# Performance work log

Measured on AMD Instinct MI355X. Metric: run time of the kernel, lower is better.

Reference implementation:

```python
import jax, jax.numpy as jnp
import numpy as np

NEG = -9e15  # kept for fidelity though mask is unused in original forward

def setup_inputs() -> dict:
    key = jax.random.key(0)
    k1, k2, k3 = jax.random.split(key, 3)
    N, Fin, Fout = 8192, 512, 256
    x = jax.random.normal(k1, (N, Fin), dtype=jnp.float32)
    # xavier_uniform with gain=1.414 ~ U(-b, b), b = gain*sqrt(6/(fan_in+fan_out))
    bW = 1.414 * np.sqrt(6.0 / (Fin + Fout))
    W = jax.random.uniform(k2, (Fin, Fout), minval=-bW, maxval=bW, dtype=jnp.float32)
    ba = 1.414 * np.sqrt(6.0 / (2 * Fout + 1))
    a = jax.random.uniform(k3, (2 * Fout, 1), minval=-ba, maxval=ba, dtype=jnp.float32)
    return {"x": x, "W": W, "a": a}

def reference(x, W, a):
    # h: [N, Fout]
    h = x @ W
    Fout = h.shape[1]
    # Algebraic decomposition of additive score: e_ij = relu(a1.h_i + a2.h_j)
    a1, a2 = a[:Fout, 0], a[Fout:, 0]  # [Fout], [Fout]
    f = h @ a1  # [N] contribution of row node i
    g = h @ a2  # [N] contribution of col node j
    e = jax.nn.relu(f[:, None] + g[None, :])  # [N, N]
    attention = jax.nn.softmax(e, axis=1)
    h_prime = attention @ h  # [N, Fout]
    return jax.nn.elu(h_prime)
```

## Files before the change

### kernel.cpp

```cpp
#include <hip/hip_runtime.h>
#include <math.h>

#define NROWS 8192
#define FIN   512
#define FOUT  256
#define NCHUNK 512
#define CHROWS 16

typedef _Float16 f16;
typedef _Float16 f16x8 __attribute__((ext_vector_type(8)));
typedef float    f32x4 __attribute__((ext_vector_type(4)));

__global__ __launch_bounds__(256) void prep(const float* __restrict__ x,
                                            const float* __restrict__ W,
                                            f16* __restrict__ xh,
                                            f16* __restrict__ Wt,
                                            float* __restrict__ fg) {
    const int b = blockIdx.x, t = threadIdx.x;
    if (b < 256) {
        const size_t base = (size_t)b * 16384;
#pragma unroll 4
        for (int i = 0; i < 16; ++i) {
            const size_t idx = base + (size_t)i * 1024 + t * 4;
            float4 v = *(const float4*)&x[idx];
            union { f16 h[4]; ushort4 u; } cv;
            cv.h[0] = (f16)v.x; cv.h[1] = (f16)v.y;
            cv.h[2] = (f16)v.z; cv.h[3] = (f16)v.w;
            *(ushort4*)&xh[idx] = cv.u;
        }
    } else {
        const int n = b - 256;
        Wt[(size_t)n * FIN + t]       = (f16)W[(size_t)t * FOUT + n];
        Wt[(size_t)n * FIN + t + 256] = (f16)W[(size_t)(t + 256) * FOUT + n];
        if (n < 64) fg[n * 256 + t] = 0.f;
    }
}

__global__ __launch_bounds__(256) void gemm_fg(const f16* __restrict__ xh,
                                               const f16* __restrict__ Wt,
                                               const float* __restrict__ a,
                                               f16* __restrict__ h,
                                               float* __restrict__ f,
                                               float* __restrict__ g) {
    __shared__ __align__(16) f16 As[64][136];
    __shared__ __align__(16) f16 Bs[64][136];
    __shared__ float sf[2][64], sg[2][64];
    const int tid = threadIdx.x;
    const int n0 = blockIdx.x * 64;
    const int m0 = blockIdx.y * 64;
    const int srow = tid >> 2, sseg = (tid & 3) * 8;
    const int w = tid >> 6, lane = tid & 63;
    const int wm = (w & 1) * 32, wn = (w >> 1) * 32;
    const int l15 = lane & 15, quad = lane >> 4;

    f16x8 pa[4], pb[4];
#pragma unroll
    for (int j = 0; j < 4; ++j) {
        pa[j] = *(const f16x8*)&xh[(size_t)(m0 + srow) * FIN + j * 32 + sseg];
        pb[j] = *(const f16x8*)&Wt[(size_t)(n0 + srow) * FIN + j * 32 + sseg];
    }

    f32x4 acc[2][2] = {};
    for (int k0 = 0; k0 < FIN; k0 += 128) {
        __syncthreads();
#pragma unroll
        for (int j = 0; j < 4; ++j) {
            *(f16x8*)&As[srow][j * 32 + sseg] = pa[j];
            *(f16x8*)&Bs[srow][j * 32 + sseg] = pb[j];
        }
        __syncthreads();
        if (k0 + 128 < FIN) {
#pragma unroll
            for (int j = 0; j < 4; ++j) {
                pa[j] = *(const f16x8*)&xh[(size_t)(m0 + srow) * FIN + k0 + 128 + j * 32 + sseg];
                pb[j] = *(const f16x8*)&Wt[(size_t)(n0 + srow) * FIN + k0 + 128 + j * 32 + sseg];
            }
        }
#pragma unroll
        for (int kk = 0; kk < 4; ++kk) {
            f16x8 af[2], bf[2];
#pragma unroll
            for (int ti = 0; ti < 2; ++ti)
                af[ti] = *(const f16x8*)&As[wm + ti * 16 + l15][kk * 32 + quad * 8];
#pragma unroll
            for (int tj = 0; tj < 2; ++tj)
                bf[tj] = *(const f16x8*)&Bs[wn + tj * 16 + l15][kk * 32 + quad * 8];
#pragma unroll
            for (int ti = 0; ti < 2; ++ti)
#pragma unroll
                for (int tj = 0; tj < 2; ++tj)
                    acc[ti][tj] = __builtin_amdgcn_mfma_f32_16x16x32_f16(af[ti], bf[tj], acc[ti][tj], 0, 0, 0);
        }
    }
#pragma unroll
    for (int ti = 0; ti < 2; ++ti)
#pragma unroll
        for (int tj = 0; tj < 2; ++tj) {
            const int col = n0 + wn + tj * 16 + l15;
#pragma unroll
            for (int r = 0; r < 4; ++r) {
                const int row = m0 + wm + ti * 16 + quad * 4 + r;
                h[(size_t)row * FOUT + col] = (f16)acc[ti][tj][r];
            }
        }
    const float a1c0 = a[n0 + wn + l15];
    const float a1c1 = a[n0 + wn + 16 + l15];
    const float a2c0 = a[FOUT + n0 + wn + l15];
    const float a2c1 = a[FOUT + n0 + wn + 16 + l15];
    const int wnIdx = w >> 1;
#pragma unroll
    for (int ti = 0; ti < 2; ++ti) {
        float pf[4], pg[4];
#pragma unroll
        for (int r = 0; r < 4; ++r) {
            pf[r] = acc[ti][0][r] * a1c0 + acc[ti][1][r] * a1c1;
            pg[r] = acc[ti][0][r] * a2c0 + acc[ti][1][r] * a2c1;
        }
#pragma unroll
        for (int off = 8; off >= 1; off >>= 1)
#pragma unroll
            for (int r = 0; r < 4; ++r) {
                pf[r] += __shfl_xor(pf[r], off, 16);
                pg[r] += __shfl_xor(pg[r], off, 16);
            }
        if (l15 == 0)
#pragma unroll
            for (int r = 0; r < 4; ++r) {
                sf[wnIdx][wm + ti * 16 + quad * 4 + r] = pf[r];
                sg[wnIdx][wm + ti * 16 + quad * 4 + r] = pg[r];
            }
    }
    __syncthreads();
    if (tid < 64) {
        atomicAdd(&f[m0 + tid], sf[0][tid] + sf[1][tid]);
        atomicAdd(&g[m0 + tid], sg[0][tid] + sg[1][tid]);
    }
}

__global__ __launch_bounds__(256) void rank_scatter(const float* __restrict__ g,
                                                    float* __restrict__ gs,
                                                    int* __restrict__ perm) {
    const int t = threadIdx.x;
    const int jl = t & 31;
    const int seg = t >> 5;
    const int j = blockIdx.x * 32 + jl;
    const float gj = g[j];
    const int base = seg * (NROWS / 8);
    int cnt = 0;
    for (int r = 0; r < NROWS / 8; r += 4) {
        const float4 v = *(const float4*)&g[base + r];
        const int i0 = base + r;
        cnt += (v.x < gj) || (v.x == gj && (i0 + 0) < j);
        cnt += (v.y < gj) || (v.y == gj && (i0 + 1) < j);
        cnt += (v.z < gj) || (v.z == gj && (i0 + 2) < j);
        cnt += (v.w < gj) || (v.w == gj && (i0 + 3) < j);
    }
    __shared__ int part[8][32];
    part[seg][jl] = cnt;
    __syncthreads();
    if (seg == 0) {
        int rank = 0;
#pragma unroll
        for (int s = 0; s < 8; ++s) rank += part[s][jl];
        gs[rank] = gj;
        perm[rank] = j;
    }
}

__global__ __launch_bounds__(256) void scan_pass1(const f16* __restrict__ h,
                                                  const int* __restrict__ perm,
                                                  const float* __restrict__ gs,
                                                  const float* __restrict__ f,
                                                  float* __restrict__ c0,
                                                  float* __restrict__ c1,
                                                  float* __restrict__ c1s,
                                                  int* __restrict__ n0arr) {
    const int b = blockIdx.x, c = threadIdx.x;
    if (b < NCHUNK) {
        const int base = b * CHROWS;
        __shared__ int p[CHROWS];
        __shared__ float wl[CHROWS];
        if (c < CHROWS) {
            p[c] = perm[base + c];
            wl[c] = expf(gs[base + c] - gs[NROWS - 1]);
        }
        __syncthreads();
        float s0 = 0.f, s1 = 0.f;
        for (int r = 0; r < CHROWS; ++r) {
            float v = (float)h[(size_t)p[r] * FOUT + c];
            s0 += v;
            s1 += wl[r] * v;
        }
        c0[b * FOUT + c] = s0;
        c1[b * FOUT + c] = s1;
        if (c == 0) {
            float t = 0.f;
            for (int r = 0; r < CHROWS; ++r) t += wl[r];
            c1s[b] = t;
        }
    } else {
        const int i = (b - NCHUNK) * 256 + c;
        const float tt = -f[i];
        int lo = 0, hi = NROWS;
        while (lo < hi) {
            int mid = (lo + hi) >> 1;
            if (gs[mid] <= tt) lo = mid + 1; else hi = mid;
        }
        n0arr[i] = lo;
    }
}

__global__ __launch_bounds__(256) void scan_pass2(const float* __restrict__ c0,
                                                  const float* __restrict__ c1,
                                                  const float* __restrict__ c1s,
                                                  float* __restrict__ o0,
                                                  float* __restrict__ o1,
                                                  float* __restrict__ o1s) {
    const int b = blockIdx.x, t = threadIdx.x;
    __shared__ float sb[256];
    if (b < 256) {
        const float e0 = c0[(2 * t) * FOUT + b];
        const float e1 = c0[(2 * t + 1) * FOUT + b];
        const float local = e0 + e1;
        sb[t] = local;
        __syncthreads();
        for (int off = 1; off < 256; off <<= 1) {
            float add = (t >= off) ? sb[t - off] : 0.f;
            __syncthreads();
            sb[t] += add;
            __syncthreads();
        }
        const float ex = sb[t] - local;
        o0[(2 * t) * FOUT + b] = ex;
        o0[(2 * t + 1) * FOUT + b] = ex + e0;
    } else if (b < 512) {
        const int col = b - 256;
        const float e0 = c1[(2 * t) * FOUT + col];
        const float e1 = c1[(2 * t + 1) * FOUT + col];
        const float local = e0 + e1;
        sb[t] = local;
        __syncthreads();
        for (int off = 1; off < 256; off <<= 1) {
            float add = (t + off < 256) ? sb[t + off] : 0.f;
            __syncthreads();
            sb[t] += add;
            __syncthreads();
        }
        const float exs = sb[t] - local;
        o1[(2 * t) * FOUT + col] = exs + e1;
        o1[(2 * t + 1) * FOUT + col] = exs;
    } else {
        const float e0 = c1s[2 * t];
        const float e1 = c1s[2 * t + 1];
        const float local = e0 + e1;
        sb[t] = local;
        __syncthreads();
        for (int off = 1; off < 256; off <<= 1) {
            float add = (t + off < 256) ? sb[t + off] : 0.f;
            __syncthreads();
            sb[t] += add;
            __syncthreads();
        }
        const float exs = sb[t] - local;
        o1s[2 * t] = exs + e1;
        o1s[2 * t + 1] = exs;
    }
}

__global__ __launch_bounds__(256) void scan_pass3(const f16* __restrict__ h,
                                                  const int* __restrict__ perm,
                                                  const float* __restrict__ gs,
                                                  const float* __restrict__ o0,
                                                  const float* __restrict__ o1,
                                                  const float* __restrict__ o1s,
                                                  f16* __restrict__ P0,
                                                  f16* __restrict__ S1,
                                                  float* __restrict__ S1s) {
    const int k = blockIdx.x, c = threadIdx.x;
    const int base = k * CHROWS;
    __shared__ int p[CHROWS];
    __shared__ float wl[CHROWS];
    if (c < CHROWS) {
        p[c] = perm[base + c];
        wl[c] = expf(gs[base + c] - gs[NROWS - 1]);
    }
    __syncthreads();
    float run0 = o0[k * FOUT + c];
    for (int r = 0; r < CHROWS; ++r) {
        P0[(size_t)(base + r) * FOUT + c] = (f16)run0;
        run0 += (float)h[(size_t)p[r] * FOUT + c];
    }
    float run1 = o1[k * FOUT + c];
    for (int r = CHROWS - 1; r >= 0; --r) {
        run1 += wl[r] * (float)h[(size_t)p[r] * FOUT + c];
        S1[(size_t)(base + r) * FOUT + c] = (f16)run1;
    }
    if (c == 0) {
        float rs = o1s[k];
        for (int r = CHROWS - 1; r >= 0; --r) { rs += wl[r]; S1s[base + r] = rs; }
    }
    if (k == NCHUNK - 1) {
        P0[(size_t)NROWS * FOUT + c] = (f16)run0;
        S1[(size_t)NROWS * FOUT + c] = (f16)0.f;
        if (c == 0) S1s[NROWS] = 0.f;
    }
}

__global__ __launch_bounds__(256) void final_kernel(const float* __restrict__ f,
                                                    const float* __restrict__ gs,
                                                    const int* __restrict__ n0arr,
                                                    const f16* __restrict__ P0,
                                                    const f16* __restrict__ S1,
                                                    const float* __restrict__ S1s,
                                                    float* __restrict__ out) {
    const int b = blockIdx.x, c = threadIdx.x;
    const float gm = gs[NROWS - 1];
#pragma unroll
    for (int rr = 0; rr < 4; ++rr) {
        const int i = b * 4 + rr;
        const float fi = f[i];
        const int n0 = n0arr[i];
        const float m = fmaxf(0.f, fi + gm);
        const float A = expf(-m);
        const float B = expf(fi + gm - m);
        const float denom = A * (float)n0 + B * S1s[n0];
        const float numer = A * (float)P0[(size_t)n0 * FOUT + c]
                          + B * (float)S1[(size_t)n0 * FOUT + c];
        const float v = numer / denom;
        out[(size_t)i * FOUT + c] = v > 0.f ? v : expm1f(v);
    }
}

extern "C" void kernel_launch(void* const* d_in, const int* in_sizes, int n_in,
                              void* d_out, int out_size, void* d_ws, size_t ws_size,
                              hipStream_t stream) {
    (void)in_sizes; (void)n_in; (void)out_size; (void)ws_size;
    const float* x = (const float*)d_in[0];
    const float* W = (const float*)d_in[1];
    const float* a = (const float*)d_in[2];
    float* out = (float*)d_out;

    char* ws = (char*)d_ws;
    size_t off = 0;
    auto alloc = [&](size_t bytes) -> void* {
        void* p = ws + off;
        off += (bytes + 255) & ~(size_t)255;
        return p;
    };
    f16*   xh   = (f16*)alloc((size_t)NROWS * FIN * 2);
    f16*   Wt   = (f16*)alloc((size_t)FOUT * FIN * 2);
    f16*   h    = (f16*)alloc((size_t)NROWS * FOUT * 2);
    f16*   P0   = (f16*)alloc((size_t)(NROWS + 1) * FOUT * 2);
    f16*   S1   = (f16*)alloc((size_t)(NROWS + 1) * FOUT * 2);
    float* fg   = (float*)alloc(2 * NROWS * 4);
    float* f    = fg;
    float* g    = fg + NROWS;
    float* gs   = (float*)alloc(NROWS * 4);
    int*   perm = (int*)alloc(NROWS * 4);
    int*   n0arr= (int*)alloc(NROWS * 4);
    float* c0   = (float*)alloc(NCHUNK * FOUT * 4);
    float* c1   = (float*)alloc(NCHUNK * FOUT * 4);
    float* o0   = (float*)alloc(NCHUNK * FOUT * 4);
    float* o1   = (float*)alloc(NCHUNK * FOUT * 4);
    float* c1s  = (float*)alloc(NCHUNK * 4);
    float* o1s  = (float*)alloc(NCHUNK * 4);
    float* S1s  = (float*)alloc((NROWS + 1) * 4);

    prep<<<512, 256, 0, stream>>>(x, W, xh, Wt, fg);
    gemm_fg<<<dim3(FOUT / 64, NROWS / 64), 256, 0, stream>>>(xh, Wt, a, h, f, g);
    rank_scatter<<<NROWS / 32, 256, 0, stream>>>(g, gs, perm);
    scan_pass1<<<NCHUNK + 32, 256, 0, stream>>>(h, perm, gs, f, c0, c1, c1s, n0arr);
    scan_pass2<<<513, 256, 0, stream>>>(c0, c1, c1s, o0, o1, o1s);
    scan_pass3<<<NCHUNK, 256, 0, stream>>>(h, perm, gs, o0, o1, o1s, P0, S1, S1s);
    final_kernel<<<NROWS / 4, 256, 0, stream>>>(f, gs, n0arr, P0, S1, S1s, out);
}
```

Before: 135.3 us.

## Fuse post-GEMM rank, scan and output kernels into one persistent kernel with grid barriers

Replaces five separate launches (rank scatter, three scan passes, final output) with a single 512-block kernel that separates the phases with software grid barriers built on atomic counters. The barrier counters are reset in the prep kernel. The binary search for n0 moves into the final phase, so the n0arr buffer goes away. The aim is to remove per-launch overhead and the tail gaps between small kernels. In exchange it depends on all 512 blocks being co-resident, and spin-waiting on the barriers adds latency.

New measurement: 380.4 us. 2.81x slower.

```diff
diff --git a/kernel.cpp b/kernel.cpp
--- a/kernel.cpp
+++ b/kernel.cpp
@@ -6,6 +6,7 @@
 #define FOUT  256
 #define NCHUNK 512
 #define CHROWS 16
+#define NBLK  512
 
 typedef _Float16 f16;
 typedef _Float16 f16x8 __attribute__((ext_vector_type(8)));
@@ -15,7 +16,8 @@
                                             const float* __restrict__ W,
                                             f16* __restrict__ xh,
                                             f16* __restrict__ Wt,
-                                            float* __restrict__ fg) {
+                                            float* __restrict__ fg,
+                                            int* __restrict__ bar) {
     const int b = blockIdx.x, t = threadIdx.x;
     if (b < 256) {
         const size_t base = (size_t)b * 16384;
@@ -33,6 +35,7 @@
         Wt[(size_t)n * FIN + t]       = (f16)W[(size_t)t * FOUT + n];
         Wt[(size_t)n * FIN + t + 256] = (f16)W[(size_t)(t + 256) * FOUT + n];
         if (n < 64) fg[n * 256 + t] = 0.f;
+        if (n == 64 && t < 8) bar[t] = 0;
     }
 }
 
@@ -137,197 +140,193 @@
     }
 }
 
-__global__ __launch_bounds__(256) void rank_scatter(const float* __restrict__ g,
-                                                    float* __restrict__ gs,
-                                                    int* __restrict__ perm) {
-    const int t = threadIdx.x;
-    const int jl = t & 31;
-    const int seg = t >> 5;
-    const int j = blockIdx.x * 32 + jl;
-    const float gj = g[j];
-    const int base = seg * (NROWS / 8);
-    int cnt = 0;
-    for (int r = 0; r < NROWS / 8; r += 4) {
-        const float4 v = *(const float4*)&g[base + r];
-        const int i0 = base + r;
-        cnt += (v.x < gj) || (v.x == gj && (i0 + 0) < j);
-        cnt += (v.y < gj) || (v.y == gj && (i0 + 1) < j);
-        cnt += (v.z < gj) || (v.z == gj && (i0 + 2) < j);
-        cnt += (v.w < gj) || (v.w == gj && (i0 + 3) < j);
-    }
-    __shared__ int part[8][32];
-    part[seg][jl] = cnt;
+__device__ __forceinline__ void grid_barrier(int* cnt) {
     __syncthreads();
-    if (seg == 0) {
-        int rank = 0;
-#pragma unroll
-        for (int s = 0; s < 8; ++s) rank += part[s][jl];
-        gs[rank] = gj;
-        perm[rank] = j;
-    }
-}
-
-__global__ __launch_bounds__(256) void scan_pass1(const f16* __restrict__ h,
-                                                  const int* __restrict__ perm,
-                                                  const float* __restrict__ gs,
-                                                  const float* __restrict__ f,
-                                                  float* __restrict__ c0,
-                                                  float* __restrict__ c1,
-                                                  float* __restrict__ c1s,
-                                                  int* __restrict__ n0arr) {
-    const int b = blockIdx.x, c = threadIdx.x;
-    if (b < NCHUNK) {
+    if (threadIdx.x == 0) {
+        __threadfence();
+        atomicAdd(cnt, 1);
+        while (__hip_atomic_load(cnt, __ATOMIC_RELAXED, __HIP_MEMORY_SCOPE_AGENT) < NBLK)
+            __builtin_amdgcn_s_sleep(1);
+    }
+    __syncthreads();
+    __threadfence();
+}
+
+__global__ __launch_bounds__(256, 2) void fused_post(
+        const f16* __restrict__ h,
+        const float* __restrict__ f, const float* __restrict__ g,
+        float* __restrict__ gs, int* __restrict__ perm,
+        float* __restrict__ c0, float* __restrict__ c1, float* __restrict__ c1s,
+        float* __restrict__ o0, float* __restrict__ o1, float* __restrict__ o1s,
+        f16* __restrict__ P0, f16* __restrict__ S1, float* __restrict__ S1s,
+        int* __restrict__ bar, float* __restrict__ out) {
+    const int b = blockIdx.x, t = threadIdx.x;
+
+    {
+        const int jl = t & 15, seg = t >> 4;
+        const int j = b * 16 + jl;
+        const float gj = g[j];
+        const int base = seg * (NROWS / 16);
+        int cnt = 0;
+        for (int r = 0; r < NROWS / 16; r += 4) {
+            const float4 v = *(const float4*)&g[base + r];
+            const int i0 = base + r;
+            cnt += (v.x < gj) || (v.x == gj && (i0 + 0) < j);
+            cnt += (v.y < gj) || (v.y == gj && (i0 + 1) < j);
+            cnt += (v.z < gj) || (v.z == gj && (i0 + 2) < j);
+            cnt += (v.w < gj) || (v.w == gj && (i0 + 3) < j);
+        }
+        __shared__ int part[16][16];
+        part[seg][jl] = cnt;
+        __syncthreads();
+        if (seg == 0) {
+            int rank = 0;
+#pragma unroll
+            for (int s = 0; s < 16; ++s) rank += part[s][jl];
+            gs[rank] = gj;
+            perm[rank] = j;
+        }
+    }
+    grid_barrier(&bar[0]);
+
+    {
         const int base = b * CHROWS;
         __shared__ int p[CHROWS];
         __shared__ float wl[CHROWS];
-        if (c < CHROWS) {
-            p[c] = perm[base + c];
-            wl[c] = expf(gs[base + c] - gs[NROWS - 1]);
+        if (t < CHROWS) {
+            p[t] = perm[base + t];
+            wl[t] = expf(gs[base + t] - gs[NROWS - 1]);
         }
         __syncthreads();
         float s0 = 0.f, s1 = 0.f;
         for (int r = 0; r < CHROWS; ++r) {
-            float v = (float)h[(size_t)p[r] * FOUT + c];
+            float v = (float)h[(size_t)p[r] * FOUT + t];
             s0 += v;
             s1 += wl[r] * v;
         }
-        c0[b * FOUT + c] = s0;
-        c1[b * FOUT + c] = s1;
-        if (c == 0) {
-            float t = 0.f;
-            for (int r = 0; r < CHROWS; ++r) t += wl[r];
-            c1s[b] = t;
-        }
-    } else {
-        const int i = (b - NCHUNK) * 256 + c;
-        const float tt = -f[i];
-        int lo = 0, hi = NROWS;
-        while (lo < hi) {
-            int mid = (lo + hi) >> 1;
-            if (gs[mid] <= tt) lo = mid + 1; else hi = mid;
-        }
-        n0arr[i] = lo;
-    }
-}
-
-__global__ __launch_bounds__(256) void scan_pass2(const float* __restrict__ c0,
-                                                  const float* __restrict__ c1,
-                                                  const float* __restrict__ c1s,
-                                                  float* __restrict__ o0,
-                                                  float* __restrict__ o1,
-                                                  float* __restrict__ o1s) {
-    const int b = blockIdx.x, t = threadIdx.x;
-    __shared__ float sb[256];
-    if (b < 256) {
-        const float e0 = c0[(2 * t) * FOUT + b];
-        const float e1 = c0[(2 * t + 1) * FOUT + b];
-        const float local = e0 + e1;
-        sb[t] = local;
-        __syncthreads();
-        for (int off = 1; off < 256; off <<= 1) {
-            float add = (t >= off) ? sb[t - off] : 0.f;
+        c0[b * FOUT + t] = s0;
+        c1[b * FOUT + t] = s1;
+        if (t == 0) {
+            float tt = 0.f;
+            for (int r = 0; r < CHROWS; ++r) tt += wl[r];
+            c1s[b] = tt;
+        }
+    }
+    grid_barrier(&bar[1]);
+
+    {
+        __shared__ float sb[256];
+        if (b < 256) {
+            const float e0 = c0[(2 * t) * FOUT + b];
+            const float e1 = c0[(2 * t + 1) * FOUT + b];
+            const float local = e0 + e1;
+            sb[t] = local;
             __syncthreads();
-            sb[t] += add;
+            for (int off = 1; off < 256; off <<= 1) {
+                float add = (t >= off) ? sb[t - off] : 0.f;
+                __syncthreads();
+                sb[t] += add;
+                __syncthreads();
+            }
+            const float ex = sb[t] - local;
+            o0[(2 * t) * FOUT + b] = ex;
+            o0[(2 * t + 1) * FOUT + b] = ex + e0;
+            if (b == 0) {
+                const float s0 = c1s[2 * t];
+                const float s1v = c1s[2 * t + 1];
+                const float loc2 = s0 + s1v;
+                __syncthreads();
+                sb[t] = loc2;
+                __syncthreads();
+                for (int off = 1; off < 256; off <<= 1) {
+                    float add = (t + off < 256) ? sb[t + off] : 0.f;
+                    __syncthreads();
+                    sb[t] += add;
+                    __syncthreads();
+                }
+                const float exs = sb[t] - loc2;
+                o1s[2 * t] = exs + s1v;
+                o1s[2 * t + 1] = exs;
+            }
+        } else {
+            const int col = b - 256;
+            const float e0 = c1[(2 * t) * FOUT + col];
+            const float e1 = c1[(2 * t + 1) * FOUT + col];
+            const float local = e0 + e1;
+            sb[t] = local;
             __syncthreads();
-        }
-        const float ex = sb[t] - local;
-        o0[(2 * t) * FOUT + b] = ex;
-        o0[(2 * t + 1) * FOUT + b] = ex + e0;
-    } else if (b < 512) {
-        const int col = b - 256;
-        const float e0 = c1[(2 * t) * FOUT + col];
-        const float e1 = c1[(2 * t + 1) * FOUT + col];
-        const float local = e0 + e1;
-        sb[t] = local;
-        __syncthreads();
-        for (int off = 1; off < 256; off <<= 1) {
-            float add = (t + off < 256) ? sb[t + off] : 0.f;
-            __syncthreads();
-            sb[t] += add;
-            __syncthreads();
-        }
-        const float exs = sb[t] - local;
-        o1[(2 * t) * FOUT + col] = exs + e1;
-        o1[(2 * t + 1) * FOUT + col] = exs;
-    } else {
-        const float e0 = c1s[2 * t];
-        const float e1 = c1s[2 * t + 1];
-        const float local = e0 + e1;
-        sb[t] = local;
-        __syncthreads();
-        for (int off = 1; off < 256; off <<= 1) {
-            float add = (t + off < 256) ? sb[t + off] : 0.f;
-            __syncthreads();
-            sb[t] += add;
-            __syncthreads();
-        }
-        const float exs = sb[t] - local;
-        o1s[2 * t] = exs + e1;
-        o1s[2 * t + 1] = exs;
-    }
-}
-
-__global__ __launch_bounds__(256) void scan_pass3(const f16* __restrict__ h,
-                                                  const int* __restrict__ perm,
-                                                  const float* __restrict__ gs,
-                                                  const float* __restrict__ o0,
-                                                  const float* __restrict__ o1,
-                                                  const float* __restrict__ o1s,
-                                                  f16* __restrict__ P0,
-                                                  f16* __restrict__ S1,
-                                                  float* __restrict__ S1s) {
-    const int k = blockIdx.x, c = threadIdx.x;
-    const int base = k * CHROWS;
-    __shared__ int p[CHROWS];
-    __shared__ float wl[CHROWS];
-    if (c < CHROWS) {
-        p[c] = perm[base + c];
-        wl[c] = expf(gs[base + c] - gs[NROWS - 1]);
-    }
-    __syncthreads();
-    float run0 = o0[k * FOUT + c];
-    for (int r = 0; r < CHROWS; ++r) {
-        P0[(size_t)(base + r) * FOUT + c] = (f16)run0;
-        run0 += (float)h[(size_t)p[r] * FOUT + c];
-    }
-    float run1 = o1[k * FOUT + c];
-    for (int r = CHROWS - 1; r >= 0; --r) {
-        run1 += wl[r] * (float)h[(size_t)p[r] * FOUT + c];
-        S1[(size_t)(base + r) * FOUT + c] = (f16)run1;
-    }
-    if (c == 0) {
-        float rs = o1s[k];
-        for (int r = CHROWS - 1; r >= 0; --r) { rs += wl[r]; S1s[base + r] = rs; }
-    }
-    if (k == NCHUNK - 1) {
-        P0[(size_t)NROWS * FOUT + c] = (f16)run0;
-        S1[(size_t)NROWS * FOUT + c] = (f16)0.f;
-        if (c == 0) S1s[NROWS] = 0.f;
-    }
-}
-
-__global__ __launch_bounds__(256) void final_kernel(const float* __restrict__ f,
-                                                    const float* __restrict__ gs,
-                                                    const int* __restrict__ n0arr,
-                                                    const f16* __restrict__ P0,
-                                                    const f16* __restrict__ S1,
-                                                    const float* __restrict__ S1s,
-                                                    float* __restrict__ out) {
-    const int b = blockIdx.x, c = threadIdx.x;
-    const float gm = gs[NROWS - 1];
-#pragma unroll
-    for (int rr = 0; rr < 4; ++rr) {
-        const int i = b * 4 + rr;
-        const float fi = f[i];
-        const int n0 = n0arr[i];
-        const float m = fmaxf(0.f, fi + gm);
-        const float A = expf(-m);
-        const float B = expf(fi + gm - m);
-        const float denom = A * (float)n0 + B * S1s[n0];
-        const float numer = A * (float)P0[(size_t)n0 * FOUT + c]
-                          + B * (float)S1[(size_t)n0 * FOUT + c];
-        const float v = numer / denom;
-        out[(size_t)i * FOUT + c] = v > 0.f ? v : expm1f(v);
+            for (int off = 1; off < 256; off <<= 1) {
+                float add = (t + off < 256) ? sb[t + off] : 0.f;
+                __syncthreads();
+                sb[t] += add;
+                __syncthreads();
+            }
+            const float exs = sb[t] - local;
+            o1[(2 * t) * FOUT + col] = exs + e1;
+            o1[(2 * t + 1) * FOUT + col] = exs;
+        }
+    }
+    grid_barrier(&bar[2]);
+
+    {
+        const int base = b * CHROWS;
+        __shared__ int p2[CHROWS];
+        __shared__ float wl2[CHROWS];
+        if (t < CHROWS) {
+            p2[t] = perm[base + t];
+            wl2[t] = expf(gs[base + t] - gs[NROWS - 1]);
+        }
+        __syncthreads();
+        float run0 = o0[b * FOUT + t];
+        for (int r = 0; r < CHROWS; ++r) {
+            P0[(size_t)(base + r) * FOUT + t] = (f16)run0;
+            run0 += (float)h[(size_t)p2[r] * FOUT + t];
+        }
+        float run1 = o1[b * FOUT + t];
+        for (int r = CHROWS - 1; r >= 0; --r) {
+            run1 += wl2[r] * (float)h[(size_t)p2[r] * FOUT + t];
+            S1[(size_t)(base + r) * FOUT + t] = (f16)run1;
+        }
+        if (t == 0) {
+            float rs = o1s[b];
+            for (int r = CHROWS - 1; r >= 0; --r) { rs += wl2[r]; S1s[base + r] = rs; }
+        }
+        if (b == NCHUNK - 1) {
+            P0[(size_t)NROWS * FOUT + t] = (f16)run0;
+            S1[(size_t)NROWS * FOUT + t] = (f16)0.f;
+            if (t == 0) S1s[NROWS] = 0.f;
+        }
+    }
+    grid_barrier(&bar[3]);
+
+    {
+        const float gm = gs[NROWS - 1];
+        __shared__ int sn0[16];
+        if (t < 16) {
+            const int i = b * 16 + t;
+            const float tt = -f[i];
+            int lo = 0, hi = NROWS;
+            while (lo < hi) {
+                int mid = (lo + hi) >> 1;
+                if (gs[mid] <= tt) lo = mid + 1; else hi = mid;
+            }
+            sn0[t] = lo;
+        }
+        __syncthreads();
+#pragma unroll 4
+        for (int rr = 0; rr < 16; ++rr) {
+            const int i = b * 16 + rr;
+            const float fi = f[i];
+            const int n0 = sn0[rr];
+            const float m = fmaxf(0.f, fi + gm);
+            const float A = expf(-m);
+            const float B = expf(fi + gm - m);
+            const float denom = A * (float)n0 + B * S1s[n0];
+            const float numer = A * (float)P0[(size_t)n0 * FOUT + t]
+                              + B * (float)S1[(size_t)n0 * FOUT + t];
+            const float v = numer / denom;
+            out[(size_t)i * FOUT + t] = v > 0.f ? v : expm1f(v);
+        }
     }
 }
 
@@ -357,7 +356,6 @@
     float* g    = fg + NROWS;
     float* gs   = (float*)alloc(NROWS * 4);
     int*   perm = (int*)alloc(NROWS * 4);
-    int*   n0arr= (int*)alloc(NROWS * 4);
     float* c0   = (float*)alloc(NCHUNK * FOUT * 4);
     float* c1   = (float*)alloc(NCHUNK * FOUT * 4);
     float* o0   = (float*)alloc(NCHUNK * FOUT * 4);
@@ -365,12 +363,10 @@
     float* c1s  = (float*)alloc(NCHUNK * 4);
     float* o1s  = (float*)alloc(NCHUNK * 4);
     float* S1s  = (float*)alloc((NROWS + 1) * 4);
-
-    prep<<<512, 256, 0, stream>>>(x, W, xh, Wt, fg);
+    int*   bar  = (int*)alloc(8 * 4);
+
+    prep<<<512, 256, 0, stream>>>(x, W, xh, Wt, fg, bar);
     gemm_fg<<<dim3(FOUT / 64, NROWS / 64), 256, 0, stream>>>(xh, Wt, a, h, f, g);
-    rank_scatter<<<NROWS / 32, 256, 0, stream>>>(g, gs, perm);
-    scan_pass1<<<NCHUNK + 32, 256, 0, stream>>>(h, perm, gs, f, c0, c1, c1s, n0arr);
-    scan_pass2<<<513, 256, 0, stream>>>(c0, c1, c1s, o0, o1, o1s);
-    scan_pass3<<<NCHUNK, 256, 0, stream>>>(h, perm, gs, o0, o1, o1s, P0, S1, S1s);
-    final_kernel<<<NROWS / 4, 256, 0, stream>>>(f, gs, n0arr, P0, S1, S1s, out);
-}
+    fused_post<<<NBLK, 256, 0, stream>>>(h, f, g, gs, perm, c0, c1, c1s,
+                                         o0, o1, o1s, P0, S1, S1s, bar, out);
+}
```
